# Kernel tuning notes

Measured on AMD Instinct MI355X. Metric: run time of the kernel, lower is better.

Reference implementation:

```python
import jax, jax.numpy as jnp
import numpy as np
from jax import lax

H = 1024
D = 128
T = 64  # n_step + n_middle


def gru_cell(x, h, w_ih, w_hh, b_ih, b_hh):
    # torch.nn.GRUCell gate order: r, z, n
    gi = x @ w_ih.T + b_ih
    gh = h @ w_hh.T + b_hh
    ir, iz, i_n = jnp.split(gi, 3, axis=-1)
    hr, hz, h_n = jnp.split(gh, 3, axis=-1)
    r = jax.nn.sigmoid(ir + hr)
    z = jax.nn.sigmoid(iz + hz)
    n = jnp.tanh(i_n + r * h_n)
    return (1.0 - z) * n + z * h


def decoder(z_seq, z8, n1, w_init, b_init, wi1, wh1, bi1, bh1, wi2, wh2, bi2, bh2, w_out, b_out):
    B = z_seq.shape[0]
    out0 = jnp.zeros((B, D), z_seq.dtype).at[:, -1].set(1.0)
    h0 = z8 @ w_init.T + b_init              # [B, H]
    h1 = jnp.zeros_like(h0)                  # replaced at i == 0
    xs = (jnp.arange(T), jnp.swapaxes(z_seq, 0, 1))  # ([T], [T, B, D])

    def step(carry, x):
        h0, h1, out = carry
        i, z_i = x
        inp = jnp.where(i <= n1 - 1, z_i, out)
        h0n = gru_cell(inp, h0, wi1, wh1, bi1, bh1)
        h1 = jnp.where(i == 0, h0n, h1)
        h1n = gru_cell(h0n, h1, wi2, wh2, bi2, bh2)
        out = h1n @ w_out.T + b_out          # [B, 128]
        return (h0n, h1n, out), out

    _, outs = lax.scan(step, (h0, h1, out0), xs)  # [T, B, 128]
    return jnp.swapaxes(outs[n1 - 1:], 0, 1)      # [B, T-n1+1, 128]


def _p(key, shape):
    return jax.random.normal(key, shape, dtype=jnp.float32) * 0.02


def setup_inputs() -> dict:
    key = jax.random.key(0)
    ks = jax.random.split(key, 32)
    B = 2048
    inp = {
        'zp': jax.random.normal(ks[0], (B, T, D), jnp.float32),
        'zr': jax.random.normal(ks[1], (B, T, D), jnp.float32),
        'zp8': jax.random.normal(ks[2], (B, D), jnp.float32),
        'zr8': jax.random.normal(ks[3], (B, D), jnp.float32),
        'n1': 16,
        'n2': 48,
    }
    # GRU cells 1..4: (w_ih [3H, in], w_hh [3H, H], b_ih [3H], b_hh [3H])
    for j, name in enumerate(['1', '2', '3', '4']):
        in_dim = D if name in ('1', '3') else H
        inp['wi' + name] = _p(ks[4 + 4 * j], (3 * H, in_dim))
        inp['wh' + name] = _p(ks[5 + 4 * j], (3 * H, H))
        inp['bi' + name] = _p(ks[6 + 4 * j], (3 * H,))
        inp['bh' + name] = _p(ks[7 + 4 * j], (3 * H,))
    inp['w_init0'] = _p(ks[20], (H, D)); inp['b_init0'] = _p(ks[21], (H,))
    inp['w_init1'] = _p(ks[22], (H, D)); inp['b_init1'] = _p(ks[23], (H,))
    inp['w_out0'] = _p(ks[24], (D, H)); inp['b_out0'] = _p(ks[25], (D,))
    inp['w_out1'] = _p(ks[26], (D, H)); inp['b_out1'] = _p(ks[27], (D,))
    return inp


def reference(zp, zr, zp8, zr8, n1, n2,
              wi1, wh1, bi1, bh1, wi2, wh2, bi2, bh2,
              wi3, wh3, bi3, bh3, wi4, wh4, bi4, bh4,
              w_init0, b_init0, w_init1, b_init1,
              w_out0, b_out0, w_out1, b_out1):
    z_r = decoder(zr, zr8, n1, w_init0, b_init0, wi1, wh1, bi1, bh1,
                  wi2, wh2, bi2, bh2, w_out0, b_out0)
    z_p = decoder(zp, zp8, n1, w_init1, b_init1, wi3, wh3, bi3, bh3,
                  wi4, wh4, bi4, bh4, w_out1, b_out1)
    return (z_p, z_r)
```

## Files before the change

### kernel.cpp

```cpp
#include <hip/hip_runtime.h>

typedef unsigned short u16;
typedef unsigned int u32;
typedef __attribute__((ext_vector_type(8))) short short8;
typedef __attribute__((ext_vector_type(4))) float f32x4;

#define DEV __device__ __forceinline__
#define SB0() __builtin_amdgcn_sched_barrier(0)

DEV u16 f2bf(float f){
  u32 u = __builtin_bit_cast(u32, f);
  u += 0x7fffu + ((u >> 16) & 1u);
  return (u16)(u >> 16);
}
DEV float sigm(float x){ return 1.f / (1.f + __expf(-x)); }
DEV float tanh_(float x){ return 2.f / (1.f + __expf(-2.f * x)) - 1.f; }

DEV void gl_lds16(const void* g, void* l){
  __builtin_amdgcn_global_load_lds(
      (const __attribute__((address_space(1))) u32*)g,
      (__attribute__((address_space(3))) u32*)l, 16, 0, 0);
}

#define MFMA16(A,B,C) __builtin_amdgcn_mfma_f32_16x16x32_bf16(A, B, C, 0, 0, 0)

__global__ void pack_w_kernel(const float* __restrict__ wi, const float* __restrict__ wh,
                              u16* __restrict__ dst, int Ki, int Kh, int nrows){
  const int KT = Ki + Kh;
  const long n = (long)nrows * KT;
  for (long idx = (long)blockIdx.x * blockDim.x + threadIdx.x; idx < n;
       idx += (long)gridDim.x * blockDim.x){
    int r = (int)(idx / KT), c = (int)(idx % KT);
    float v = (c < Ki) ? wi[(long)r * Ki + c] : wh[(long)r * Kh + (c - Ki)];
    dst[idx] = f2bf(v);
  }
}

struct InitA { const float* z8; const float* wini; const float* bini; float* h0f; u16* h0bf; };

__global__ __launch_bounds__(256)
void init_kernel(InitA A0, InitA A1){
  const InitA& a = (blockIdx.z == 0) ? A0 : A1;
  __shared__ float lz[64][128];
  const int tid = threadIdx.x;
  const int rb = blockIdx.x * 64, ub = blockIdx.y * 128;
  {
    const int row = tid >> 2, q = tid & 3;
    const float4* p = (const float4*)(a.z8 + (long)(rb + row) * 128 + q * 32);
    float4* dst = (float4*)&lz[row][q * 32];
    #pragma unroll
    for (int j = 0; j < 8; ++j) dst[j] = p[j];
  }
  __syncthreads();
  const int u = ub + (tid & 127);
  const int rg = tid >> 7;
  float acc[32];
  #pragma unroll
  for (int r = 0; r < 32; ++r) acc[r] = 0.f;
  for (int k = 0; k < 128; k += 4){
    float4 w4 = *(const float4*)&a.wini[(long)u * 128 + k];
    #pragma unroll
    for (int r = 0; r < 32; ++r){
      float4 z4 = *(const float4*)&lz[rg * 32 + r][k];
      acc[r] += w4.x * z4.x + w4.y * z4.y + w4.z * z4.z + w4.w * z4.w;
    }
  }
  const float b = a.bini[u];
  #pragma unroll
  for (int r = 0; r < 32; ++r){
    const long row = rb + rg * 32 + r;
    const float v = acc[r] + b;
    a.h0f[row * 1024 + u] = v;
    a.h0bf[row * 1024 + u] = f2bf(v);
  }
}

struct CellA {
  const u16* W;
  const float* bi; const float* bh;
  const float* afz; const float* afo;
  const u16* ab1; const u16* ab2;
  const float* holdr; float* holdw; u16* hbfw;
};

template<int CELL>
__global__ __attribute__((amdgpu_waves_per_eu(2, 2))) __launch_bounds__(512)
void cell_kernel(CellA A0, CellA A1, const int* dn1, int step){
  constexpr int KTOT = (CELL == 1) ? 1152 : 2048;
  constexpr int KT = KTOT / 64;
  constexpr int NI_STEPS = (CELL == 1) ? 2 : 16;

  __shared__ u16 lA[2][256 * 64];
  __shared__ u16 lB[2][192 * 64];

  const CellA& a = (blockIdx.y == 0) ? A0 : A1;
  const int tid = threadIdx.x;
  const int lane = tid & 63;
  const int wv = tid >> 6;
  const int wm = wv >> 1;
  const int wn = wv & 1;
  const int bid = blockIdx.x;
  const int inner = bid >> 3;
  const int m_idx = ((bid >> 2) & 1) * 4 + (inner & 3);
  const int n_idx = (bid & 3) * 4 + (inner >> 2);
  const int brow = m_idx * 256;
  const int u0 = n_idx * 64;

  f32x4 aR[4][2] = {}; f32x4 aZ[4][2] = {};
  f32x4 aNI[4][2] = {}; f32x4 aNH[4][2] = {};

  const int srow = tid >> 3;
  const int sxor8 = ((tid & 7) ^ (srow & 7)) * 8;

  auto stage = [&](int bf, int kt){
    const int k0 = kt * 64;
    const u16* ab; int kk;
    if constexpr (CELL == 1){ ab = a.ab1; kk = k0 - 128; }
    else { if (k0 < 1024){ ab = a.ab1; kk = k0; } else { ab = a.ab2; kk = k0 - 1024; } }
    #pragma unroll
    for (int j = 0; j < 4; ++j)
      gl_lds16(ab + (long)(brow + j * 64 + srow) * 1024 + kk + sxor8,
               &lA[bf][(j * 64 + wv * 8) * 64]);
    #pragma unroll
    for (int g = 0; g < 3; ++g)
      gl_lds16(a.W + (long)(g * 1024 + u0 + srow) * KTOT + k0 + sxor8,
               &lB[bf][(g * 64 + wv * 8) * 64]);
  };

  const int l15 = lane & 15;
  const int kq = lane >> 4;
  const int sx = lane & 7;

  auto read_a_ks = [&](int bf, int ks, short8 (&af)[4]){
    const int soff = (((ks * 4 + kq) ^ sx)) * 8;
    #pragma unroll
    for (int fr = 0; fr < 4; ++fr)
      af[fr] = *(const short8*)&lA[bf][(wm * 64 + fr * 16 + l15) * 64 + soff];
  };
  auto read_b_ks = [&](int bf, int g, int ks, short8 (&bg)[2]){
    const int soff = (((ks * 4 + kq) ^ sx)) * 8;
    #pragma unroll
    for (int fc = 0; fc < 2; ++fc)
      bg[fc] = *(const short8*)&lB[bf][(g * 64 + wn * 32 + fc * 16 + l15) * 64 + soff];
  };
  auto mfma8 = [&](const short8 (&af)[4], const short8 (&bg)[2], f32x4 (&A)[4][2]){
    #pragma unroll
    for (int fr = 0; fr < 4; ++fr)
      #pragma unroll
      for (int fc = 0; fc < 2; ++fc)
        A[fr][fc] = MFMA16(af[fr], bg[fc], A[fr][fc]);
  };

  int kstart;
  if constexpr (CELL == 1){
    const int n1v = *dn1;
    const float* fsrc; long fstr;
    if (step < n1v){ fsrc = a.afz; fstr = 64 * 128; }
    else           { fsrc = a.afo; fstr = 128; }
    {
      const int row = tid >> 1, half = tid & 1;
      #pragma unroll
      for (int st = 0; st < 2; ++st){
        const float* pp = fsrc + (long)(brow + row) * fstr + st * 64 + half * 32;
        #pragma unroll
        for (int q = 0; q < 4; ++q){
          float4 x = ((const float4*)pp)[2 * q];
          float4 y = ((const float4*)pp)[2 * q + 1];
          short8 o;
          o[0] = (short)f2bf(x.x); o[1] = (short)f2bf(x.y);
          o[2] = (short)f2bf(x.z); o[3] = (short)f2bf(x.w);
          o[4] = (short)f2bf(y.x); o[5] = (short)f2bf(y.y);
          o[6] = (short)f2bf(y.z); o[7] = (short)f2bf(y.w);
          const int s = half * 4 + q;
          *(short8*)&lA[st][row * 64 + ((s ^ (row & 7)) * 8)] = o;
        }
        #pragma unroll
        for (int g = 0; g < 3; ++g)
          gl_lds16(a.W + (long)(g * 1024 + u0 + srow) * KTOT + st * 64 + sxor8,
                   &lB[st][(g * 64 + wv * 8) * 64]);
      }
    }
    __syncthreads();
    #pragma unroll
    for (int st = 0; st < 2; ++st){
      short8 af0[4], af1[4], b0[2], b1[2];
      read_a_ks(st, 0, af0); read_a_ks(st, 1, af1);
      read_b_ks(st, 0, 0, b0); read_b_ks(st, 0, 1, b1);
      asm volatile("s_waitcnt lgkmcnt(0)" ::: "memory"); SB0();
      mfma8(af0, b0, aR); mfma8(af1, b1, aR);
      read_b_ks(st, 1, 0, b0); read_b_ks(st, 1, 1, b1);
      asm volatile("s_waitcnt lgkmcnt(0)" ::: "memory"); SB0();
      mfma8(af0, b0, aZ); mfma8(af1, b1, aZ);
      read_b_ks(st, 2, 0, b0); read_b_ks(st, 2, 1, b1);
      asm volatile("s_waitcnt lgkmcnt(0)" ::: "memory"); SB0();
      mfma8(af0, b0, aNI); mfma8(af1, b1, aNI);
    }
    __syncthreads();
    stage(0, 2); stage(1, 3);
    kstart = 2;
  } else {
    stage(0, 0); stage(1, 1);
    kstart = 0;
  }

  for (int kt = kstart; kt < KT; ++kt){
    const int b = kt & 1;
    if (kt < KT - 1) asm volatile("s_waitcnt vmcnt(7)" ::: "memory");
    else             asm volatile("s_waitcnt vmcnt(0)" ::: "memory");
    SB0();
    __builtin_amdgcn_s_barrier();
    SB0();
    short8 af0[4], af1[4], bR0[2], bR1[2], bZ0[2], bZ1[2], bN0[2], bN1[2];
    read_a_ks(b, 0, af0); read_b_ks(b, 0, 0, bR0); SB0();
    read_b_ks(b, 1, 0, bZ0); read_b_ks(b, 2, 0, bN0); SB0();
    read_a_ks(b, 1, af1); read_b_ks(b, 0, 1, bR1); SB0();
    asm volatile("s_waitcnt lgkmcnt(10)" ::: "memory"); SB0();
    __builtin_amdgcn_s_setprio(1);
    mfma8(af0, bR0, aR);
    __builtin_amdgcn_s_setprio(0); SB0();
    read_b_ks(b, 1, 1, bZ1); read_b_ks(b, 2, 1, bN1); SB0();
    asm volatile("s_waitcnt lgkmcnt(10)" ::: "memory"); SB0();
    __builtin_amdgcn_s_setprio(1);
    mfma8(af0, bZ0, aZ);
    if (kt < NI_STEPS) mfma8(af0, bN0, aNI); else mfma8(af0, bN0, aNH);
    __builtin_amdgcn_s_setprio(0); SB0();
    asm volatile("s_waitcnt lgkmcnt(4)" ::: "memory"); SB0();
    __builtin_amdgcn_s_setprio(1);
    mfma8(af1, bR1, aR);
    __builtin_amdgcn_s_setprio(0); SB0();
    asm volatile("s_waitcnt lgkmcnt(0)" ::: "memory"); SB0();
    __builtin_amdgcn_s_barrier();
    SB0();
    if (kt + 2 < KT) stage(b, kt + 2);
    __builtin_amdgcn_s_setprio(1);
    mfma8(af1, bZ1, aZ);
    if (kt < NI_STEPS) mfma8(af1, bN1, aNI); else mfma8(af1, bN1, aNH);
    __builtin_amdgcn_s_setprio(0);
  }

  const int rq = (lane >> 4) * 4;
  #pragma unroll
  for (int fc = 0; fc < 2; ++fc){
    const int u = u0 + wn * 32 + fc * 16 + l15;
    const float br = a.bi[u] + a.bh[u];
    const float bz = a.bi[1024 + u] + a.bh[1024 + u];
    const float bni = a.bi[2048 + u];
    const float bnh = a.bh[2048 + u];
    #pragma unroll
    for (int fr = 0; fr < 4; ++fr){
      #pragma unroll
      for (int rg = 0; rg < 4; ++rg){
        const long row = brow + wm * 64 + fr * 16 + rq + rg;
        const float r = sigm(aR[fr][fc][rg] + br);
        const float z = sigm(aZ[fr][fc][rg] + bz);
        const float n = tanh_(aNI[fr][fc][rg] + bni + r * (aNH[fr][fc][rg] + bnh));
        const float hp = a.holdr[row * 1024 + u];
        const float hn = (1.f - z) * n + z * hp;
        a.holdw[row * 1024 + u] = hn;
        a.hbfw[row * 1024 + u] = f2bf(hn);
      }
    }
  }
}

struct OutA { const u16* Ah; const u16* Wo; const float* bo; float* outf; };

__global__ __launch_bounds__(256, 2)
void out_kernel(OutA A0, OutA A1, const int* dn1, int step, float* __restrict__ dout, long outhalf){
  const int n1v = *dn1;
  if (step < n1v - 1) return;
  __shared__ u16 lA[2][32 * 64];
  __shared__ u16 lB[2][128 * 64];
  const OutA& a = (blockIdx.y == 0) ? A0 : A1;
  const int tid = threadIdx.x, lane = tid & 63, wv = tid >> 6;
  const int brow = blockIdx.x * 32;
  f32x4 acc[2][2] = {};
  const int srow = tid >> 3;
  const int sxor8 = ((tid & 7) ^ (srow & 7)) * 8;

  auto stage = [&](int bf, int kt){
    const int k0 = kt * 64;
    gl_lds16(a.Ah + (long)(brow + srow) * 1024 + k0 + sxor8, &lA[bf][wv * 8 * 64]);
    #pragma unroll
    for (int j = 0; j < 4; ++j)
      gl_lds16(a.Wo + (long)(j * 32 + srow) * 1024 + k0 + sxor8,
               &lB[bf][(j * 32 + wv * 8) * 64]);
  };

  stage(0, 0); stage(1, 1);
  const int l15 = lane & 15, kq = lane >> 4, sx = lane & 7;
  for (int kt = 0; kt < 16; ++kt){
    const int b = kt & 1;
    if (kt < 15) asm volatile("s_waitcnt vmcnt(5)" ::: "memory");
    else         asm volatile("s_waitcnt vmcnt(0)" ::: "memory");
    SB0();
    __builtin_amdgcn_s_barrier();
    SB0();
    short8 af[2][2], bf2[2][2];
    #pragma unroll
    for (int ks = 0; ks < 2; ++ks){
      const int soff = (((ks * 4 + kq) ^ sx)) * 8;
      af[ks][0] = *(const short8*)&lA[b][(l15) * 64 + soff];
      af[ks][1] = *(const short8*)&lA[b][(16 + l15) * 64 + soff];
      bf2[ks][0] = *(const short8*)&lB[b][(wv * 32 + l15) * 64 + soff];
      bf2[ks][1] = *(const short8*)&lB[b][(wv * 32 + 16 + l15) * 64 + soff];
    }
    asm volatile("s_waitcnt lgkmcnt(0)" ::: "memory"); SB0();
    __builtin_amdgcn_s_barrier();
    SB0();
    if (kt + 2 < 16) stage(b, kt + 2);
    __builtin_amdgcn_s_setprio(1);
    #pragma unroll
    for (int ks = 0; ks < 2; ++ks)
      #pragma unroll
      for (int fr = 0; fr < 2; ++fr)
        #pragma unroll
        for (int fc = 0; fc < 2; ++fc)
          acc[fr][fc] = MFMA16(af[ks][fr], bf2[ks][fc], acc[fr][fc]);
    __builtin_amdgcn_s_setprio(0);
  }
  const int nst = 65 - n1v;
  const int t = step - (n1v - 1);
  const int rq = (lane >> 4) * 4;
  #pragma unroll
  for (int fc = 0; fc < 2; ++fc){
    const int u = wv * 32 + fc * 16 + l15;
    const float bo = a.bo[u];
    #pragma unroll
    for (int fr = 0; fr < 2; ++fr){
      #pragma unroll
      for (int rg = 0; rg < 4; ++rg){
        const long row = brow + fr * 16 + rq + rg;
        const float v = acc[fr][fc][rg] + bo;
        a.outf[row * 128 + u] = v;
        dout[(long)blockIdx.y * outhalf + (row * nst + t) * 128 + u] = v;
      }
    }
  }
}

extern "C" void kernel_launch(void* const* d_in, const int* in_sizes, int n_in,
                              void* d_out, int out_size, void* d_ws, size_t ws_size,
                              hipStream_t stream){
  const float* zz[2]   = { (const float*)d_in[0],  (const float*)d_in[1] };
  const float* z8[2]   = { (const float*)d_in[2],  (const float*)d_in[3] };
  const int* dn1       = (const int*)d_in[4];
  const float* wi_c1[2] = { (const float*)d_in[14], (const float*)d_in[6] };
  const float* wh_c1[2] = { (const float*)d_in[15], (const float*)d_in[7] };
  const float* bi_c1[2] = { (const float*)d_in[16], (const float*)d_in[8] };
  const float* bh_c1[2] = { (const float*)d_in[17], (const float*)d_in[9] };
  const float* wi_c2[2] = { (const float*)d_in[18], (const float*)d_in[10] };
  const float* wh_c2[2] = { (const float*)d_in[19], (const float*)d_in[11] };
  const float* bi_c2[2] = { (const float*)d_in[20], (const float*)d_in[12] };
  const float* bh_c2[2] = { (const float*)d_in[21], (const float*)d_in[13] };
  const float* wini[2]  = { (const float*)d_in[24], (const float*)d_in[22] };
  const float* bini[2]  = { (const float*)d_in[25], (const float*)d_in[23] };
  const float* wout[2]  = { (const float*)d_in[28], (const float*)d_in[26] };
  const float* bout[2]  = { (const float*)d_in[29], (const float*)d_in[27] };

  char* p = (char*)d_ws;
  auto alloc = [&](size_t bytes)->char*{
    char* q = p; p += (bytes + 255) & ~(size_t)255; return q;
  };
  u16* W1c[2]; u16* W2c[2]; u16* Woc[2];
  float* h0f[2]; float* h1f[2]; float* outf[2];
  u16* h0bf[2][2]; u16* h1bf[2][2];
  for (int d = 0; d < 2; ++d){
    W1c[d] = (u16*)alloc(3072ULL * 1152 * 2);
    W2c[d] = (u16*)alloc(3072ULL * 2048 * 2);
    Woc[d] = (u16*)alloc(128ULL * 1024 * 2);
    h0f[d] = (float*)alloc(2048ULL * 1024 * 4);
    h1f[d] = (float*)alloc(2048ULL * 1024 * 4);
    outf[d] = (float*)alloc(2048ULL * 128 * 4);
    for (int b = 0; b < 2; ++b){
      h0bf[d][b] = (u16*)alloc(2048ULL * 1024 * 2);
      h1bf[d][b] = (u16*)alloc(2048ULL * 1024 * 2);
    }
  }
  if ((size_t)(p - (char*)d_ws) > ws_size) return;

  for (int d = 0; d < 2; ++d){
    pack_w_kernel<<<dim3(1024), dim3(256), 0, stream>>>(wi_c1[d], wh_c1[d], W1c[d], 128, 1024, 3072);
    pack_w_kernel<<<dim3(1024), dim3(256), 0, stream>>>(wi_c2[d], wh_c2[d], W2c[d], 1024, 1024, 3072);
    pack_w_kernel<<<dim3(64),   dim3(256), 0, stream>>>(wout[d], wout[d], Woc[d], 1024, 0, 128);
  }
  {
    InitA I0{ z8[0], wini[0], bini[0], h0f[0], h0bf[0][0] };
    InitA I1{ z8[1], wini[1], bini[1], h0f[1], h0bf[1][0] };
    init_kernel<<<dim3(32, 8, 2), dim3(256), 0, stream>>>(I0, I1);
  }

  const long outhalf = (long)out_size / 2;

  for (int i = 0; i < 64; ++i){
    const int cur = i & 1, nxt = cur ^ 1;
    CellA c1[2], c2[2];
    for (int d = 0; d < 2; ++d){
      c1[d] = CellA{ W1c[d], bi_c1[d], bh_c1[d],
                     zz[d] + (long)i * 128, outf[d],
                     h0bf[d][cur], nullptr,
                     h0f[d], h0f[d], h0bf[d][nxt] };
      c2[d] = CellA{ W2c[d], bi_c2[d], bh_c2[d],
                     nullptr, nullptr,
                     h0bf[d][nxt], (i == 0) ? h0bf[d][nxt] : h1bf[d][cur],
                     (i == 0) ? h0f[d] : h1f[d], h1f[d], h1bf[d][nxt] };
    }
    cell_kernel<1><<<dim3(128, 2), dim3(512), 0, stream>>>(c1[0], c1[1], dn1, i);
    cell_kernel<2><<<dim3(128, 2), dim3(512), 0, stream>>>(c2[0], c2[1], dn1, i);
    OutA o0{ h1bf[0][nxt], Woc[0], bout[0], outf[0] };
    OutA o1{ h1bf[1][nxt], Woc[1], bout[1], outf[1] };
    out_kernel<<<dim3(64, 2), dim3(256), 0, stream>>>(o0, o1, dn1, i, (float*)d_out, outhalf);
  }
}
```

Measured before the change: 6.674 ms.

## Restructure GRU GEMM main loop into barrier-phased ping-pong LDS/MFMA schedule

Reorganizes the K-loop of the fused GRU cell GEMM so LDS fragment reads are split into three phases, each bracketed by workgroup barriers and full lgkmcnt waits before the MFMA groups. The global-load wait and barrier move from the top to the bottom of the iteration. The apparent aim is to interleave waves so some issue LDS reads while others run MFMAs, in a ping-pong style. In exchange it adds several extra s_barriers per iteration and drops the partial lgkmcnt overlap the old schedule had, which could serialize work.

```diff
diff --git a/kernel.cpp b/kernel.cpp
--- a/kernel.cpp
+++ b/kernel.cpp
@@ -23,6 +23,7 @@
 }
 
 #define MFMA16(A,B,C) __builtin_amdgcn_mfma_f32_16x16x32_bf16(A, B, C, 0, 0, 0)
+#define LGKM0() do{ asm volatile("s_waitcnt lgkmcnt(0)" ::: "memory"); SB0(); }while(0)
 
 __global__ void pack_w_kernel(const float* __restrict__ wi, const float* __restrict__ wh,
                               u16* __restrict__ dst, int Ki, int Kh, int nrows){
@@ -186,56 +187,60 @@
       short8 af0[4], af1[4], b0[2], b1[2];
       read_a_ks(st, 0, af0); read_a_ks(st, 1, af1);
       read_b_ks(st, 0, 0, b0); read_b_ks(st, 0, 1, b1);
-      asm volatile("s_waitcnt lgkmcnt(0)" ::: "memory"); SB0();
+      LGKM0();
       mfma8(af0, b0, aR); mfma8(af1, b1, aR);
       read_b_ks(st, 1, 0, b0); read_b_ks(st, 1, 1, b1);
-      asm volatile("s_waitcnt lgkmcnt(0)" ::: "memory"); SB0();
+      LGKM0();
       mfma8(af0, b0, aZ); mfma8(af1, b1, aZ);
       read_b_ks(st, 2, 0, b0); read_b_ks(st, 2, 1, b1);
-      asm volatile("s_waitcnt lgkmcnt(0)" ::: "memory"); SB0();
+      LGKM0();
       mfma8(af0, b0, aNI); mfma8(af1, b1, aNI);
     }
     __syncthreads();
     stage(0, 2); stage(1, 3);
+    asm volatile("s_waitcnt vmcnt(7)" ::: "memory"); SB0();
+    __builtin_amdgcn_s_barrier();
     kstart = 2;
   } else {
     stage(0, 0); stage(1, 1);
+    asm volatile("s_waitcnt vmcnt(7)" ::: "memory"); SB0();
+    __builtin_amdgcn_s_barrier();
     kstart = 0;
   }
 
   for (int kt = kstart; kt < KT; ++kt){
     const int b = kt & 1;
-    if (kt < KT - 1) asm volatile("s_waitcnt vmcnt(7)" ::: "memory");
-    else             asm volatile("s_waitcnt vmcnt(0)" ::: "memory");
-    SB0();
-    __builtin_amdgcn_s_barrier();
-    SB0();
     short8 af0[4], af1[4], bR0[2], bR1[2], bZ0[2], bZ1[2], bN0[2], bN1[2];
-    read_a_ks(b, 0, af0); read_b_ks(b, 0, 0, bR0); SB0();
-    read_b_ks(b, 1, 0, bZ0); read_b_ks(b, 2, 0, bN0); SB0();
-    read_a_ks(b, 1, af1); read_b_ks(b, 0, 1, bR1); SB0();
-    asm volatile("s_waitcnt lgkmcnt(10)" ::: "memory"); SB0();
+    read_a_ks(b, 0, af0); read_b_ks(b, 0, 0, bR0); read_b_ks(b, 1, 0, bZ0);
+    __builtin_amdgcn_s_barrier();
+    LGKM0();
     __builtin_amdgcn_s_setprio(1);
     mfma8(af0, bR0, aR);
-    __builtin_amdgcn_s_setprio(0); SB0();
-    read_b_ks(b, 1, 1, bZ1); read_b_ks(b, 2, 1, bN1); SB0();
-    asm volatile("s_waitcnt lgkmcnt(10)" ::: "memory"); SB0();
+    __builtin_amdgcn_s_setprio(0);
+    __builtin_amdgcn_s_barrier(); SB0();
+    read_b_ks(b, 2, 0, bN0); read_a_ks(b, 1, af1);
+    __builtin_amdgcn_s_barrier();
+    LGKM0();
     __builtin_amdgcn_s_setprio(1);
     mfma8(af0, bZ0, aZ);
     if (kt < NI_STEPS) mfma8(af0, bN0, aNI); else mfma8(af0, bN0, aNH);
-    __builtin_amdgcn_s_setprio(0); SB0();
-    asm volatile("s_waitcnt lgkmcnt(4)" ::: "memory"); SB0();
+    __builtin_amdgcn_s_setprio(0);
+    __builtin_amdgcn_s_barrier(); SB0();
+    read_b_ks(b, 0, 1, bR1); read_b_ks(b, 1, 1, bZ1); read_b_ks(b, 2, 1, bN1);
+    __builtin_amdgcn_s_barrier();
+    LGKM0();
     __builtin_amdgcn_s_setprio(1);
     mfma8(af1, bR1, aR);
-    __builtin_amdgcn_s_setprio(0); SB0();
-    asm volatile("s_waitcnt lgkmcnt(0)" ::: "memory"); SB0();
-    __builtin_amdgcn_s_barrier();
-    SB0();
+    __builtin_amdgcn_s_setprio(0);
+    __builtin_amdgcn_s_barrier(); SB0();
     if (kt + 2 < KT) stage(b, kt + 2);
     __builtin_amdgcn_s_setprio(1);
     mfma8(af1, bZ1, aZ);
     if (kt < NI_STEPS) mfma8(af1, bN1, aNI); else mfma8(af1, bN1, aNH);
     __builtin_amdgcn_s_setprio(0);
+    if (kt < KT - 2)       { asm volatile("s_waitcnt vmcnt(7)" ::: "memory"); SB0(); }
+    else if (kt == KT - 2) { asm volatile("s_waitcnt vmcnt(0)" ::: "memory"); SB0(); }
+    if (kt + 1 < KT) __builtin_amdgcn_s_barrier();
   }
 
   const int rq = (lane >> 4) * 4;
```

Result: slower. 7.355 ms (+10.2%).
